# Optimization experiments

Measured on AMD Instinct MI355X. Metric: run time of the kernel, lower is better.

## Reference

```python
import jax, jax.numpy as jnp
import numpy as np


def _conv(x, k, pad):
    # x: [B,1,H,W], k: [1,1,kh,kw]
    return jax.lax.conv_general_dilated(
        x, k, window_strides=(1, 1), padding=[(pad, pad), (pad, pad)],
        dimension_numbers=('NCHW', 'OIHW', 'NCHW'))


def _gauss_kernel(size=15, sigma=2.0):
    c = np.arange(size, dtype=np.float32) - size // 2
    k = np.exp(-(c[:, None] ** 2 + c[None, :] ** 2) / (2.0 * sigma ** 2))
    k = k / k.sum()
    return jnp.asarray(k, dtype=jnp.float32)[None, None]


_SOBEL_X = jnp.array([[[[-1., 0., 1.], [-2., 0., 2.], [-1., 0., 1.]]]], dtype=jnp.float32)
_SOBEL_Y = jnp.array([[[[-1., -2., -1.], [0., 0., 0.], [1., 2., 1.]]]], dtype=jnp.float32)
_GAUSS = _gauss_kernel(15, 2.0)


def _edge_density(img):
    gray = 0.299 * img[:, 0] + 0.587 * img[:, 1] + 0.114 * img[:, 2]  # [B,H,W]
    box = jnp.ones((1, 1, 5, 5), jnp.float32) / 25.0  # avg_pool2d, count_include_pad
    blurred = _conv(gray[:, None], box, 2)
    gx = _conv(blurred, _SOBEL_X, 1)
    gy = _conv(blurred, _SOBEL_Y, 1)
    mag = jnp.sqrt(gx ** 2 + gy ** 2)
    hi = mag.max() * 0.2
    lo = hi * 0.3
    edge_map = ((mag > lo) & (mag < hi)).astype(jnp.float32)
    return _conv(edge_map, _GAUSS, 7)  # [B,1,H,W]


def _color_sparsity(img):
    # Replaces the O(K*B*H*W) python loop over unique quantized colors with a
    # 32^3-bin histogram (scatter-add) and a single per-pixel gather.
    b, c, h, w = img.shape
    idx = jnp.clip(jnp.round(img * 31.0), 0, 31).astype(jnp.int32)  # [B,3,H,W]
    code = idx[:, 0] * 1024 + idx[:, 1] * 32 + idx[:, 2]  # [B,H,W]
    counts = jnp.zeros(32 * 32 * 32, jnp.float32).at[code.reshape(-1)].add(1.0)
    prob = counts[code] / float(b * h * w)  # [B,H,W]
    return (-jnp.log(prob + 1e-9) * 1.5)[:, None]  # [B,1,H,W]


def setup_inputs() -> dict:
    key = jax.random.key(0)
    img = jax.random.uniform(key, (1, 3, 3072, 3072), dtype=jnp.float32)
    return {
        'img': img,
        'alpha': jnp.asarray(0.5, dtype=jnp.float32),
        'beta': jnp.asarray(0.5, dtype=jnp.float32),
    }


def reference(img, alpha, beta):
    ed = _edge_density(img)
    cs = _color_sparsity(img)
    en = (ed - ed.min()) / (ed.max() - ed.min() + 1e-9)
    cn = (cs - cs.min()) / (cs.max() - cs.min() + 1e-9)
    return jax.nn.sigmoid(alpha * en + beta * cn)  # [B,1,H,W]
```

## Files before the change

### kernel.cpp

```cpp
#include <hip/hip_runtime.h>
#include <math.h>

#define TW 3072
#define TH 3072
#define NPIX (TW*TH)

__global__ void k_init(unsigned* scal) {
    if (threadIdx.x == 0) {
        scal[0] = 0u;
        scal[1] = 0x7F800000u;
        scal[2] = 0u;
        scal[3] = 0u;
        scal[4] = 0xFFFFFFFFu;
    }
}

__device__ __forceinline__ int qcode(float r, float g, float b) {
    int ir = min(max((int)rintf(__fmul_rn(r, 31.f)), 0), 31);
    int ig = min(max((int)rintf(__fmul_rn(g, 31.f)), 0), 31);
    int ib = min(max((int)rintf(__fmul_rn(b, 31.f)), 0), 31);
    return ir * 1024 + ig * 32 + ib;
}

__device__ __forceinline__ float grayf(float r, float g, float b) {
    return __fadd_rn(__fadd_rn(__fmul_rn(0.299f, r), __fmul_rn(0.587f, g)),
                     __fmul_rn(0.114f, b));
}

__global__ __launch_bounds__(512) void k_pre(const float4* __restrict__ img4,
                                             float4* __restrict__ gray4,
                                             ushort4* __restrict__ code4,
                                             unsigned* __restrict__ parthist) {
    __shared__ unsigned lh[16384];
    for (int t = threadIdx.x; t < 16384; t += 512) lh[t] = 0u;
    __syncthreads();
    const int total4 = NPIX / 4;
    int stride = gridDim.x * blockDim.x;
    for (int p = blockIdx.x * blockDim.x + threadIdx.x; p < total4; p += stride) {
        float4 r = img4[p], g = img4[p + total4], b = img4[p + 2 * total4];
        float4 gy;
        gy.x = grayf(r.x, g.x, b.x);
        gy.y = grayf(r.y, g.y, b.y);
        gy.z = grayf(r.z, g.z, b.z);
        gy.w = grayf(r.w, g.w, b.w);
        gray4[p] = gy;
        int c0 = qcode(r.x, g.x, b.x);
        int c1 = qcode(r.y, g.y, b.y);
        int c2 = qcode(r.z, g.z, b.z);
        int c3 = qcode(r.w, g.w, b.w);
        atomicAdd(&lh[c0 >> 1], (c0 & 1) ? 0x10000u : 1u);
        atomicAdd(&lh[c1 >> 1], (c1 & 1) ? 0x10000u : 1u);
        atomicAdd(&lh[c2 >> 1], (c2 & 1) ? 0x10000u : 1u);
        atomicAdd(&lh[c3 >> 1], (c3 & 1) ? 0x10000u : 1u);
        ushort4 cc;
        cc.x = (unsigned short)c0; cc.y = (unsigned short)c1;
        cc.z = (unsigned short)c2; cc.w = (unsigned short)c3;
        code4[p] = cc;
    }
    __syncthreads();
    unsigned* dst = parthist + (size_t)blockIdx.x * 16384;
    for (int t = threadIdx.x; t < 16384; t += 512) dst[t] = lh[t];
}

__global__ void k_reduce(const unsigned* __restrict__ parthist, unsigned* __restrict__ hist,
                         float* __restrict__ cstab, unsigned* __restrict__ scal) {
    int b = blockIdx.x * blockDim.x + threadIdx.x;
    unsigned lo = 0u, hi = 0u;
#pragma unroll 4
    for (int k = 0; k < 512; k++) {
        unsigned v = parthist[(size_t)k * 16384 + b];
        lo += v & 0xFFFFu;
        hi += v >> 16;
    }
    hist[2 * b] = lo;
    hist[2 * b + 1] = hi;
    const float N = (float)NPIX;
    cstab[2 * b]     = -logf((float)lo / N + 1e-9f) * 1.5f;
    cstab[2 * b + 1] = -logf((float)hi / N + 1e-9f) * 1.5f;
    unsigned mx = max(lo, hi);
    unsigned mn = 0xFFFFFFFFu;
    if (lo) mn = lo;
    if (hi) mn = min(mn, hi);
#pragma unroll
    for (int o = 32; o > 0; o >>= 1) {
        mx = max(mx, (unsigned)__shfl_down((int)mx, o));
        mn = min(mn, (unsigned)__shfl_down((int)mn, o));
    }
    __shared__ unsigned smx[4], smn[4];
    int lane = threadIdx.x & 63, wv = threadIdx.x >> 6;
    if (lane == 0) { smx[wv] = mx; smn[wv] = mn; }
    __syncthreads();
    if (threadIdx.x == 0) {
        unsigned a = max(max(smx[0], smx[1]), max(smx[2], smx[3]));
        unsigned c = min(min(smn[0], smn[1]), min(smn[2], smn[3]));
        atomicMax(&scal[3], a);
        atomicMin(&scal[4], c);
    }
}

__device__ __forceinline__ void blockMaxMinAtomic(float vmax, float vmin,
                                                  unsigned* pmax, unsigned* pmin) {
#pragma unroll
    for (int o = 32; o > 0; o >>= 1) {
        vmax = fmaxf(vmax, __shfl_down(vmax, o));
        vmin = fminf(vmin, __shfl_down(vmin, o));
    }
    __shared__ float smax[8], smin[8];
    int lane = threadIdx.x & 63, wv = threadIdx.x >> 6;
    if (lane == 0) { smax[wv] = vmax; smin[wv] = vmin; }
    __syncthreads();
    if (threadIdx.x == 0) {
        int nw = blockDim.x >> 6;
        float a = smax[0], b = smin[0];
        for (int k = 1; k < nw; k++) { a = fmaxf(a, smax[k]); b = fminf(b, smin[k]); }
        if (pmax) atomicMax(pmax, __float_as_uint(a));
        if (pmin) atomicMin(pmin, __float_as_uint(b));
    }
}

#define BS_W 256
#define BS_H 24
#define GTW 264
#define GTH 30
#define BLW 260
#define BLH 26
__global__ __launch_bounds__(512) void k_boxsobel(const float* __restrict__ g,
                                                  float* __restrict__ mag,
                                                  unsigned* __restrict__ scal) {
    __shared__ float GT[GTH * GTW];
    __shared__ float BL[BLH * BLW];
    int tid = threadIdx.x;
    int x0 = blockIdx.x * BS_W;
    int y0 = blockIdx.y * BS_H;
    for (int t = tid; t < GTH * GTW; t += 512) {
        int ly = t / GTW, lx = t - ly * GTW;
        int y = y0 - 3 + ly, x = x0 - 3 + lx;
        GT[t] = ((unsigned)y < TH && (unsigned)x < TW) ? g[(size_t)y * TW + x] : 0.f;
    }
    __syncthreads();
    for (int t = tid; t < BLH * 65; t += 512) {
        int by = t / 65, gx = t - by * 65;
        int c0 = gx * 4;
        float acc[4] = {0.f, 0.f, 0.f, 0.f};
#pragma unroll
        for (int a = 0; a < 5; a++) {
            const float* rp = &GT[(by + a) * GTW + c0];
            float4 A = *(const float4*)rp;
            float4 B = *(const float4*)(rp + 4);
            float v[8] = {A.x, A.y, A.z, A.w, B.x, B.y, B.z, B.w};
#pragma unroll
            for (int j = 0; j < 4; j++)
#pragma unroll
                for (int b = 0; b < 5; b++)
                    acc[j] = __fadd_rn(acc[j], __fmul_rn(v[j + b], 0.04f));
        }
        int yb = y0 - 1 + by;
        float4 o;
        float* ov = (float*)&o;
#pragma unroll
        for (int j = 0; j < 4; j++) {
            int xb = x0 - 1 + c0 + j;
            ov[j] = ((unsigned)yb < TH && (unsigned)xb < TW) ? acc[j] : 0.f;
        }
        *(float4*)&BL[by * BLW + c0] = o;
    }
    __syncthreads();
    float tmax = 0.f;
    for (int t = tid; t < 24 * 64; t += 512) {
        int oy = t >> 6, gx = t & 63;
        int c0 = gx * 4;
        float v[3][6];
#pragma unroll
        for (int a = 0; a < 3; a++) {
            const float* rp = &BL[(oy + a) * BLW + c0];
            float4 P = *(const float4*)rp;
            float2 Q = *(const float2*)(rp + 4);
            v[a][0] = P.x; v[a][1] = P.y; v[a][2] = P.z; v[a][3] = P.w;
            v[a][4] = Q.x; v[a][5] = Q.y;
        }
        float4 mo;
        float* mv = (float*)&mo;
#pragma unroll
        for (int j = 0; j < 4; j++) {
            float gxv = 0.f;
            gxv = __fadd_rn(gxv, __fmul_rn(-1.f, v[0][j + 0]));
            gxv = __fadd_rn(gxv, v[0][j + 2]);
            gxv = __fadd_rn(gxv, __fmul_rn(-2.f, v[1][j + 0]));
            gxv = __fadd_rn(gxv, __fmul_rn(2.f, v[1][j + 2]));
            gxv = __fadd_rn(gxv, __fmul_rn(-1.f, v[2][j + 0]));
            gxv = __fadd_rn(gxv, v[2][j + 2]);
            float gyv = 0.f;
            gyv = __fadd_rn(gyv, __fmul_rn(-1.f, v[0][j + 0]));
            gyv = __fadd_rn(gyv, __fmul_rn(-2.f, v[0][j + 1]));
            gyv = __fadd_rn(gyv, __fmul_rn(-1.f, v[0][j + 2]));
            gyv = __fadd_rn(gyv, v[2][j + 0]);
            gyv = __fadd_rn(gyv, __fmul_rn(2.f, v[2][j + 1]));
            gyv = __fadd_rn(gyv, v[2][j + 2]);
            float m = sqrtf(__fadd_rn(__fmul_rn(gxv, gxv), __fmul_rn(gyv, gyv)));
            mv[j] = m;
            tmax = fmaxf(tmax, m);
        }
        *(float4*)&mag[(size_t)(y0 + oy) * TW + x0 + c0] = mo;
    }
    blockMaxMinAtomic(tmax, 0.f, &scal[0], nullptr);
}

#define GS_W 256
#define GS_H 32
#define EW32 68
#define E_H 46
__global__ __launch_bounds__(512) void k_gauss(const float* __restrict__ mag,
                                               float* __restrict__ ed,
                                               const unsigned* __restrict__ scal,
                                               unsigned* __restrict__ scalw) {
    __shared__ float wt[15];
    __shared__ unsigned E8[E_H * EW32];
    __shared__ float EH[E_H * GS_W];
    if (threadIdx.x == 0) {
        float w[15];
        float s = 0.f;
        for (int t = 0; t < 15; t++) {
            int c = t - 7;
            w[t] = expf(-(float)(c * c) * 0.125f);
            s += w[t];
        }
        for (int t = 0; t < 15; t++) wt[t] = w[t] / s;
    }
    __syncthreads();
    float magmax = __uint_as_float(scal[0]);
    float hi = __fmul_rn(magmax, 0.2f);
    float lo = __fmul_rn(hi, 0.3f);
    int tid = threadIdx.x;
    int x0 = blockIdx.x * GS_W;
    int y0 = blockIdx.y * GS_H;
    for (int t = tid; t < E_H * EW32; t += 512) {
        int ly = t / EW32, w = t - ly * EW32;
        int y = y0 - 7 + ly;
        bool yin = (unsigned)y < TH;
        const float* mrow = mag + (size_t)y * TW;
        int xbase = x0 - 7 + w * 4;
        unsigned pack = 0u;
#pragma unroll
        for (int j = 0; j < 4; j++) {
            int x = xbase + j;
            float m = (yin && (unsigned)x < TW) ? mrow[x] : 0.f;
            if (m > lo && m < hi) pack |= 1u << (8 * j);
        }
        E8[t] = pack;
    }
    __syncthreads();
    for (int t = tid; t < E_H * 64; t += 512) {
        int ly = t >> 6, gx = t & 63;
        int c0 = gx * 4;
        const unsigned* row = &E8[ly * EW32 + gx];
        unsigned w0 = row[0], w1 = row[1], w2 = row[2], w3 = row[3], w4 = row[4];
        float e[20];
#pragma unroll
        for (int j = 0; j < 4; j++) {
            e[j]      = (float)((w0 >> (8 * j)) & 0xffu);
            e[4 + j]  = (float)((w1 >> (8 * j)) & 0xffu);
            e[8 + j]  = (float)((w2 >> (8 * j)) & 0xffu);
            e[12 + j] = (float)((w3 >> (8 * j)) & 0xffu);
            e[16 + j] = (float)((w4 >> (8 * j)) & 0xffu);
        }
        float4 o;
        float* ov = (float*)&o;
#pragma unroll
        for (int j = 0; j < 4; j++) {
            float acc = 0.f;
#pragma unroll
            for (int k = 0; k < 15; k++) acc = fmaf(e[j + k], wt[k], acc);
            ov[j] = acc;
        }
        *(float4*)&EH[ly * GS_W + c0] = o;
    }
    __syncthreads();
    float tmin = INFINITY, tmax = 0.f;
    for (int t = tid; t < GS_H * 64; t += 512) {
        int r = t >> 6, gx = t & 63;
        int c0 = gx * 4;
        float a0 = 0.f, a1 = 0.f, a2 = 0.f, a3 = 0.f;
#pragma unroll
        for (int k = 0; k < 15; k++) {
            float4 v = *(const float4*)&EH[(r + k) * GS_W + c0];
            a0 = fmaf(v.x, wt[k], a0);
            a1 = fmaf(v.y, wt[k], a1);
            a2 = fmaf(v.z, wt[k], a2);
            a3 = fmaf(v.w, wt[k], a3);
        }
        float4 o; o.x = a0; o.y = a1; o.z = a2; o.w = a3;
        *(float4*)&ed[(size_t)(y0 + r) * TW + x0 + c0] = o;
        tmin = fminf(tmin, fminf(fminf(a0, a1), fminf(a2, a3)));
        tmax = fmaxf(tmax, fmaxf(fmaxf(a0, a1), fmaxf(a2, a3)));
    }
    blockMaxMinAtomic(tmax, tmin, &scalw[2], &scalw[1]);
}

__global__ void k_final(float4* __restrict__ io4, const ushort4* __restrict__ code4,
                        const float* __restrict__ cstab, const unsigned* __restrict__ scal,
                        const float* __restrict__ alphap, const float* __restrict__ betap) {
    float edmin = __uint_as_float(scal[1]);
    float edmax = __uint_as_float(scal[2]);
    float edrange = edmax - edmin + 1e-9f;
    const float N = (float)NPIX;
    float csmin = -logf((float)scal[3] / N + 1e-9f) * 1.5f;
    float csmax = -logf((float)scal[4] / N + 1e-9f) * 1.5f;
    float csrange = csmax - csmin + 1e-9f;
    float alpha = *alphap, beta = *betap;
    const int total4 = NPIX / 4;
    int stride = gridDim.x * blockDim.x;
    for (int p = blockIdx.x * blockDim.x + threadIdx.x; p < total4; p += stride) {
        float4 ed = io4[p];
        ushort4 cc = code4[p];
        float edv[4] = {ed.x, ed.y, ed.z, ed.w};
        unsigned short cv[4] = {cc.x, cc.y, cc.z, cc.w};
        float ov[4];
#pragma unroll
        for (int t = 0; t < 4; t++) {
            float en = (edv[t] - edmin) / edrange;
            float cs = cstab[cv[t]];
            float cn = (cs - csmin) / csrange;
            float x = alpha * en + beta * cn;
            ov[t] = 1.f / (1.f + expf(-x));
        }
        float4 o;
        o.x = ov[0]; o.y = ov[1]; o.z = ov[2]; o.w = ov[3];
        io4[p] = o;
    }
}

extern "C" void kernel_launch(void* const* d_in, const int* in_sizes, int n_in,
                              void* d_out, int out_size, void* d_ws, size_t ws_size,
                              hipStream_t stream) {
    const float* img = (const float*)d_in[0];
    const float* alphap = (const float*)d_in[1];
    const float* betap = (const float*)d_in[2];
    float* out = (float*)d_out;

    char* ws = (char*)d_ws;
    unsigned* scal = (unsigned*)ws;
    unsigned* hist = (unsigned*)(ws + 1024);
    float* cstab = (float*)(ws + 1024 + 131072);
    float* G = (float*)(ws + 524288);
    float* M = (float*)(ws + 524288 + (size_t)NPIX * 4);
    unsigned short* code = (unsigned short*)(ws + 524288 + (size_t)NPIX * 8);
    unsigned* parthist = (unsigned*)M;

    hipLaunchKernelGGL(k_init, dim3(1), dim3(64), 0, stream, scal);
    hipLaunchKernelGGL(k_pre, dim3(512), dim3(512), 0, stream,
                       (const float4*)img, (float4*)G, (ushort4*)code, parthist);
    hipLaunchKernelGGL(k_reduce, dim3(64), dim3(256), 0, stream, parthist, hist, cstab, scal);
    hipLaunchKernelGGL(k_boxsobel, dim3(TW / BS_W, TH / BS_H), dim3(512), 0, stream,
                       G, M, scal);
    hipLaunchKernelGGL(k_gauss, dim3(TW / GS_W, TH / GS_H), dim3(512), 0, stream,
                       M, out, scal, scal);
    hipLaunchKernelGGL(k_final, dim3(2304), dim3(256), 0, stream, (float4*)out,
                       (const ushort4*)code, cstab, scal, alphap, betap);
}
```

Baseline: 345.7 us.

## Bit-pack edge map in gauss kernel, fold init into pre-pass, unroll pre loop

```diff
diff --git a/kernel.cpp b/kernel.cpp
--- a/kernel.cpp
+++ b/kernel.cpp
@@ -5,49 +5,78 @@
 #define TH 3072
 #define NPIX (TW*TH)
 
-__global__ void k_init(unsigned* scal) {
-    if (threadIdx.x == 0) {
+__device__ __forceinline__ int qcode(float r, float g, float b) {
+    int ir = min(max((int)rintf(__fmul_rn(r, 31.f)), 0), 31);
+    int ig = min(max((int)rintf(__fmul_rn(g, 31.f)), 0), 31);
+    int ib = min(max((int)rintf(__fmul_rn(b, 31.f)), 0), 31);
+    return ir * 1024 + ig * 32 + ib;
+}
+
+__device__ __forceinline__ float grayf(float r, float g, float b) {
+    return __fadd_rn(__fadd_rn(__fmul_rn(0.299f, r), __fmul_rn(0.587f, g)),
+                     __fmul_rn(0.114f, b));
+}
+
+__global__ __launch_bounds__(512) void k_pre(const float4* __restrict__ img4,
+                                             float4* __restrict__ gray4,
+                                             ushort4* __restrict__ code4,
+                                             unsigned* __restrict__ parthist,
+                                             unsigned* __restrict__ scal) {
+    if (blockIdx.x == 0 && threadIdx.x == 0) {
         scal[0] = 0u;
         scal[1] = 0x7F800000u;
         scal[2] = 0u;
         scal[3] = 0u;
         scal[4] = 0xFFFFFFFFu;
     }
-}
-
-__device__ __forceinline__ int qcode(float r, float g, float b) {
-    int ir = min(max((int)rintf(__fmul_rn(r, 31.f)), 0), 31);
-    int ig = min(max((int)rintf(__fmul_rn(g, 31.f)), 0), 31);
-    int ib = min(max((int)rintf(__fmul_rn(b, 31.f)), 0), 31);
-    return ir * 1024 + ig * 32 + ib;
-}
-
-__device__ __forceinline__ float grayf(float r, float g, float b) {
-    return __fadd_rn(__fadd_rn(__fmul_rn(0.299f, r), __fmul_rn(0.587f, g)),
-                     __fmul_rn(0.114f, b));
-}
-
-__global__ __launch_bounds__(512) void k_pre(const float4* __restrict__ img4,
-                                             float4* __restrict__ gray4,
-                                             ushort4* __restrict__ code4,
-                                             unsigned* __restrict__ parthist) {
     __shared__ unsigned lh[16384];
     for (int t = threadIdx.x; t < 16384; t += 512) lh[t] = 0u;
     __syncthreads();
     const int total4 = NPIX / 4;
-    int stride = gridDim.x * blockDim.x;
-    for (int p = blockIdx.x * blockDim.x + threadIdx.x; p < total4; p += stride) {
+    const int stride = 512 * 512;
+    int base = blockIdx.x * 512 + threadIdx.x;
+#pragma unroll
+    for (int k = 0; k < 8; k += 2) {
+        int p = base + k * stride;
+        int q = p + stride;
+        float4 r0 = img4[p], g0 = img4[p + total4], b0 = img4[p + 2 * total4];
+        float4 r1 = img4[q], g1 = img4[q + total4], b1 = img4[q + 2 * total4];
+        float4 gy0, gy1;
+        gy0.x = grayf(r0.x, g0.x, b0.x); gy0.y = grayf(r0.y, g0.y, b0.y);
+        gy0.z = grayf(r0.z, g0.z, b0.z); gy0.w = grayf(r0.w, g0.w, b0.w);
+        gy1.x = grayf(r1.x, g1.x, b1.x); gy1.y = grayf(r1.y, g1.y, b1.y);
+        gy1.z = grayf(r1.z, g1.z, b1.z); gy1.w = grayf(r1.w, g1.w, b1.w);
+        gray4[p] = gy0;
+        gray4[q] = gy1;
+        int c0 = qcode(r0.x, g0.x, b0.x), c1 = qcode(r0.y, g0.y, b0.y);
+        int c2 = qcode(r0.z, g0.z, b0.z), c3 = qcode(r0.w, g0.w, b0.w);
+        int d0 = qcode(r1.x, g1.x, b1.x), d1 = qcode(r1.y, g1.y, b1.y);
+        int d2 = qcode(r1.z, g1.z, b1.z), d3 = qcode(r1.w, g1.w, b1.w);
+        atomicAdd(&lh[c0 >> 1], (c0 & 1) ? 0x10000u : 1u);
+        atomicAdd(&lh[c1 >> 1], (c1 & 1) ? 0x10000u : 1u);
+        atomicAdd(&lh[c2 >> 1], (c2 & 1) ? 0x10000u : 1u);
+        atomicAdd(&lh[c3 >> 1], (c3 & 1) ? 0x10000u : 1u);
+        atomicAdd(&lh[d0 >> 1], (d0 & 1) ? 0x10000u : 1u);
+        atomicAdd(&lh[d1 >> 1], (d1 & 1) ? 0x10000u : 1u);
+        atomicAdd(&lh[d2 >> 1], (d2 & 1) ? 0x10000u : 1u);
+        atomicAdd(&lh[d3 >> 1], (d3 & 1) ? 0x10000u : 1u);
+        ushort4 cc, dd;
+        cc.x = (unsigned short)c0; cc.y = (unsigned short)c1;
+        cc.z = (unsigned short)c2; cc.w = (unsigned short)c3;
+        dd.x = (unsigned short)d0; dd.y = (unsigned short)d1;
+        dd.z = (unsigned short)d2; dd.w = (unsigned short)d3;
+        code4[p] = cc;
+        code4[q] = dd;
+    }
+    {
+        int p = base + 8 * stride;
         float4 r = img4[p], g = img4[p + total4], b = img4[p + 2 * total4];
         float4 gy;
-        gy.x = grayf(r.x, g.x, b.x);
-        gy.y = grayf(r.y, g.y, b.y);
-        gy.z = grayf(r.z, g.z, b.z);
-        gy.w = grayf(r.w, g.w, b.w);
+        gy.x = grayf(r.x, g.x, b.x); gy.y = grayf(r.y, g.y, b.y);
+        gy.z = grayf(r.z, g.z, b.z); gy.w = grayf(r.w, g.w, b.w);
         gray4[p] = gy;
-        int c0 = qcode(r.x, g.x, b.x);
-        int c1 = qcode(r.y, g.y, b.y);
-        int c2 = qcode(r.z, g.z, b.z);
-        int c3 = qcode(r.w, g.w, b.w);
+        int c0 = qcode(r.x, g.x, b.x), c1 = qcode(r.y, g.y, b.y);
+        int c2 = qcode(r.z, g.z, b.z), c3 = qcode(r.w, g.w, b.w);
         atomicAdd(&lh[c0 >> 1], (c0 & 1) ? 0x10000u : 1u);
         atomicAdd(&lh[c1 >> 1], (c1 & 1) ? 0x10000u : 1u);
         atomicAdd(&lh[c2 >> 1], (c2 & 1) ? 0x10000u : 1u);
@@ -206,15 +235,15 @@
 }
 
 #define GS_W 256
-#define GS_H 32
-#define EW32 68
-#define E_H 46
+#define GS_H 48
+#define E_H 62
+#define EWB 10
 __global__ __launch_bounds__(512) void k_gauss(const float* __restrict__ mag,
                                                float* __restrict__ ed,
                                                const unsigned* __restrict__ scal,
                                                unsigned* __restrict__ scalw) {
     __shared__ float wt[15];
-    __shared__ unsigned E8[E_H * EW32];
+    __shared__ unsigned E8[E_H * EWB];
     __shared__ float EH[E_H * GS_W];
     if (threadIdx.x == 0) {
         float w[15];
@@ -233,18 +262,19 @@
     int tid = threadIdx.x;
     int x0 = blockIdx.x * GS_W;
     int y0 = blockIdx.y * GS_H;
-    for (int t = tid; t < E_H * EW32; t += 512) {
-        int ly = t / EW32, w = t - ly * EW32;
+    for (int t = tid; t < E_H * EWB; t += 512) {
+        int ly = t / EWB, w = t - ly * EWB;
         int y = y0 - 7 + ly;
         bool yin = (unsigned)y < TH;
         const float* mrow = mag + (size_t)y * TW;
-        int xbase = x0 - 7 + w * 4;
+        int xbase = x0 - 7 + w * 32;
         unsigned pack = 0u;
 #pragma unroll
-        for (int j = 0; j < 4; j++) {
+        for (int j = 0; j < 32; j++) {
+            int lx = w * 32 + j;
             int x = xbase + j;
-            float m = (yin && (unsigned)x < TW) ? mrow[x] : 0.f;
-            if (m > lo && m < hi) pack |= 1u << (8 * j);
+            float m = (yin && lx < 270 && (unsigned)x < TW) ? mrow[x] : 0.f;
+            if (m > lo && m < hi) pack |= 1u << j;
         }
         E8[t] = pack;
     }
@@ -252,17 +282,13 @@
     for (int t = tid; t < E_H * 64; t += 512) {
         int ly = t >> 6, gx = t & 63;
         int c0 = gx * 4;
-        const unsigned* row = &E8[ly * EW32 + gx];
-        unsigned w0 = row[0], w1 = row[1], w2 = row[2], w3 = row[3], w4 = row[4];
-        float e[20];
-#pragma unroll
-        for (int j = 0; j < 4; j++) {
-            e[j]      = (float)((w0 >> (8 * j)) & 0xffu);
-            e[4 + j]  = (float)((w1 >> (8 * j)) & 0xffu);
-            e[8 + j]  = (float)((w2 >> (8 * j)) & 0xffu);
-            e[12 + j] = (float)((w3 >> (8 * j)) & 0xffu);
-            e[16 + j] = (float)((w4 >> (8 * j)) & 0xffu);
-        }
+        int w0 = c0 >> 5, sh = c0 & 31;
+        unsigned lo32 = E8[ly * EWB + w0];
+        unsigned hi32 = E8[ly * EWB + w0 + 1];
+        unsigned long long win = (((unsigned long long)hi32 << 32) | lo32) >> sh;
+        float e[18];
+#pragma unroll
+        for (int j = 0; j < 18; j++) e[j] = (float)((unsigned)(win >> j) & 1u);
         float4 o;
         float* ov = (float*)&o;
 #pragma unroll
@@ -346,9 +372,8 @@
     unsigned short* code = (unsigned short*)(ws + 524288 + (size_t)NPIX * 8);
     unsigned* parthist = (unsigned*)M;
 
-    hipLaunchKernelGGL(k_init, dim3(1), dim3(64), 0, stream, scal);
     hipLaunchKernelGGL(k_pre, dim3(512), dim3(512), 0, stream,
-                       (const float4*)img, (float4*)G, (ushort4*)code, parthist);
+                       (const float4*)img, (float4*)G, (ushort4*)code, parthist, scal);
     hipLaunchKernelGGL(k_reduce, dim3(64), dim3(256), 0, stream, parthist, hist, cstab, scal);
     hipLaunchKernelGGL(k_boxsobel, dim3(TW / BS_W, TH / BS_H), dim3(512), 0, stream,
                        G, M, scal);
```

New measurement: 344.7 us. Within noise of the previous version (-0.3%).
